# Kernel tuning notes

Measured on AMD Instinct MI355X. Metric: run time of the kernel, lower is better.

## Reference

```python
import jax, jax.numpy as jnp
import numpy as np

NF, NH1, NH21, NH22, NCLS = 6, 128, 128, 128, 3
OBS_X, OBS_Y, OBS_Z, R = 10.0, 10.0, 9.0, 7.0
BATCH = 131072


def setup_inputs() -> dict:
    key = jax.random.key(0)
    ks = jax.random.split(key, 16)
    def lin(kw, kb, fan_in, fan_out):
        bound = 1.0 / np.sqrt(fan_in)
        w = jax.random.uniform(kw, (fan_out, fan_in), jnp.float32, -bound, bound)
        b = jax.random.uniform(kb, (fan_out,), jnp.float32, -bound, bound)
        return w, b
    fc1_w, fc1_b = lin(ks[0], ks[1], NF, NH1)
    fc21_w, fc21_b = lin(ks[2], ks[3], NH1, NH21)
    fc22_w, fc22_b = lin(ks[4], ks[5], NH1, NH22)
    fcm1_w, fcm1_b = lin(ks[6], ks[7], NH21, NH21)
    fcm2_w, fcm2_b = lin(ks[8], ks[9], NH22, NH22)
    fc31_w, fc31_b = lin(ks[10], ks[11], NH21, NCLS)
    fc32_w, fc32_b = lin(ks[12], ks[13], NH22, 2)
    x = jax.random.normal(ks[14], (BATCH, NF), jnp.float32)
    mean = jnp.array([10.0, 0.0, 10.0, 0.0, 9.0, 0.0], jnp.float32)
    std = jnp.array([5.0, 2.0, 5.0, 2.0, 5.0, 2.0], jnp.float32)
    return {"x": x, "mean": mean, "std": std,
            "fc1_w": fc1_w, "fc1_b": fc1_b,
            "fc21_w": fc21_w, "fc21_b": fc21_b,
            "fc22_w": fc22_w, "fc22_b": fc22_b,
            "fcm1_w": fcm1_w, "fcm1_b": fcm1_b,
            "fcm2_w": fcm2_w, "fcm2_b": fcm2_b,
            "fc31_w": fc31_w, "fc31_b": fc31_b,
            "fc32_w": fc32_w, "fc32_b": fc32_b,
            "sgn": 1}


def _forward(x, mean, std, fc1_w, fc1_b, fc21_w, fc21_b, fc22_w, fc22_b,
             fcm1_w, fcm1_b, fcm2_w, fcm2_b, fc31_w, fc31_b, fc32_w, fc32_b):
    x0 = x * std + mean                                   # de-normalized state [B,6]
    h = jnp.tanh(x @ fc1_w.T + fc1_b)                     # [B,NH1]
    x21 = jnp.tanh(h @ fc21_w.T + fc21_b)
    x22 = jnp.tanh(h @ fc22_w.T + fc22_b)
    x21 = jnp.tanh(x21 @ fcm1_w.T + fcm1_b)
    x22 = jnp.tanh(x22 @ fcm2_w.T + fcm2_b)
    x31 = x21 @ fc31_w.T + fc31_b                         # QP linear term p, [B,3]
    x32 = 4.0 * jax.nn.sigmoid(x22 @ fc32_w.T + fc32_b)   # HOCBF penalties, [B,2]

    # higher-order CBF terms
    px, vx, py, vy, pz, vz = (x0[:, i] for i in range(6))
    dx, dy, dz = px - OBS_X, py - OBS_Y, pz - OBS_Z
    barrier = dx**4 + dy**4 + dz**4 - R**4
    barrier_dot = 4.0 * (dx**3 * vx + dy**3 * vy + dz**3 * vz)
    Lf2b = 12.0 * (dx**2 * vx**2 + dy**2 * vy**2 + dz**2 * vz**2)
    G = -4.0 * jnp.stack([dx**3, dy**3, dz**3], axis=-1)  # [B,3], single constraint G u <= h
    hvec = Lf2b + (x32[:, 0] + x32[:, 1]) * barrier_dot + x32[:, 0] * x32[:, 1] * barrier  # [B]

    # QP: min 0.5 u^T u + x31^T u  s.t.  G u <= h  (Q = I, one constraint)
    # Closed-form KKT: u = -x31 - lam*G, lam = max(0, (G @ (-x31) - h) / (G @ G))
    u_unc = -x31
    Gu = jnp.sum(G * u_unc, axis=-1)                      # [B]
    GG = jnp.sum(G * G, axis=-1)                          # [B]
    lam = jnp.maximum(Gu - hvec, 0.0) / GG
    u = u_unc - lam[:, None] * G                          # [B,3]
    return u


def reference(x, mean, std, fc1_w, fc1_b, fc21_w, fc21_b, fc22_w, fc22_b,
              fcm1_w, fcm1_b, fcm2_w, fcm2_b, fc31_w, fc31_b, fc32_w, fc32_b, sgn):
    return _forward(x, mean, std, fc1_w, fc1_b, fc21_w, fc21_b, fc22_w, fc22_b,
                    fcm1_w, fcm1_b, fcm2_w, fcm2_b, fc31_w, fc31_b, fc32_w, fc32_b)
```

## Files before the change

### kernel.cpp

```cpp
#include <hip/hip_runtime.h>

typedef _Float16 half8 __attribute__((ext_vector_type(8)));
typedef _Float16 half4_t __attribute__((ext_vector_type(4)));
typedef float float4_t __attribute__((ext_vector_type(4)));

#define NH 128
#define SB 64
#define NT 256

#define OFF_W1   0
#define OFF_W21  4096
#define OFF_W22  20480
#define OFF_WM1  36864
#define OFF_WM2  53248
#define OFF_W4   69632
#define WS_ELEMS 70272

__device__ __forceinline__ float fast_tanh(float x) {
  x = fminf(15.f, fmaxf(-15.f, x));
  float e = __builtin_amdgcn_exp2f(x * 2.8853900817779268f);
  return (e - 1.f) * __builtin_amdgcn_rcpf(e + 1.f);
}
__device__ __forceinline__ float sigmoid4(float z) {
  z = fminf(30.f, fmaxf(-30.f, z));
  float e = __builtin_amdgcn_exp2f(-z * 1.4426950408889634f);
  return 4.f * __builtin_amdgcn_rcpf(1.f + e);
}

__global__ void prepack(const float* __restrict__ w1, const float* __restrict__ w21,
                        const float* __restrict__ w22, const float* __restrict__ wm1,
                        const float* __restrict__ wm2, const float* __restrict__ w31,
                        const float* __restrict__ w32, _Float16* __restrict__ ws) {
  for (int i = blockIdx.x * blockDim.x + threadIdx.x; i < WS_ELEMS;
       i += gridDim.x * blockDim.x) {
    float v;
    if (i < OFF_W21) {
      int t = i;
      int j = t & 7, c = t >> 3, l16 = c & 15, t1 = c >> 4;
      int k8 = t1 & 3, mt = t1 >> 2;
      int row = mt * 16 + l16, k = k8 * 8 + j;
      v = (k < 6) ? w1[row * 6 + k] : 0.f;
    } else if (i < OFF_W4) {
      int t = i - OFF_W21;
      int m = t >> 14; t &= 16383;
      const float* src = (m == 0) ? w21 : (m == 1) ? w22 : (m == 2) ? wm1 : wm2;
      int j = t & 7, c = t >> 3, l16 = c & 15, t1 = c >> 4;
      int k8 = t1 & 15, mt = t1 >> 4;
      v = src[(mt * 16 + l16) * 128 + k8 * 8 + j];
    } else {
      int t = i - OFF_W4;
      int r = t >> 7, k = t & 127;
      v = (r < 3) ? w31[r * 128 + k] : w32[(r - 3) * 128 + k];
    }
    ws[i] = (_Float16)v;
  }
}

template <int K>
__device__ __forceinline__ void gemm_layer(const _Float16* __restrict__ Wg,
                                           const _Float16* __restrict__ inB,
                                           const float* __restrict__ biasL,
                                           _Float16* __restrict__ outB) {
  constexpr int KC = K / 8;
  constexpr int KS = K / 32;
  const int tid  = threadIdx.x;
  const int wv   = tid >> 6;
  const int lane = tid & 63;
  const int quad = lane >> 4;
  const int l16  = lane & 15;
  const int mt0 = wv * 2, mt1 = mt0 + 1;

  half8 a0[KS], a1[KS];
#pragma unroll
  for (int kk = 0; kk < KS; ++kk) {
    a0[kk] = *(const half8*)(Wg + ((mt0 * KC + kk * 4 + quad) * 16 + l16) * 8);
    a1[kk] = *(const half8*)(Wg + ((mt1 * KC + kk * 4 + quad) * 16 + l16) * 8);
  }
  float4_t acc0[4], acc1[4];
#pragma unroll
  for (int nt = 0; nt < 4; ++nt) {
    acc0[nt] = (float4_t){0.f, 0.f, 0.f, 0.f};
    acc1[nt] = (float4_t){0.f, 0.f, 0.f, 0.f};
  }
#pragma unroll
  for (int kk = 0; kk < KS; ++kk) {
#pragma unroll
    for (int nt = 0; nt < 4; ++nt) {
      half8 b = *(const half8*)(inB + (kk * 4 + quad) * 512 + (nt * 16 + l16) * 8);
      acc0[nt] = __builtin_amdgcn_mfma_f32_16x16x32_f16(a0[kk], b, acc0[nt], 0, 0, 0);
      acc1[nt] = __builtin_amdgcn_mfma_f32_16x16x32_f16(a1[kk], b, acc1[nt], 0, 0, 0);
    }
  }
  const float4_t bv0 = *(const float4_t*)(biasL + mt0 * 16 + quad * 4);
  const float4_t bv1 = *(const float4_t*)(biasL + mt1 * 16 + quad * 4);
  const int ob0 = mt0 * 16 + quad * 4;
  const int ob1 = mt1 * 16 + quad * 4;
#pragma unroll
  for (int nt = 0; nt < 4; ++nt) {
    const int s = nt * 16 + l16;
    half4_t h0, h1;
#pragma unroll
    for (int r = 0; r < 4; ++r) {
      h0[r] = (_Float16)fast_tanh(acc0[nt][r] + bv0[r]);
      h1[r] = (_Float16)fast_tanh(acc1[nt][r] + bv1[r]);
    }
    *(half4_t*)(outB + (ob0 >> 3) * 512 + s * 8 + (ob0 & 7)) = h0;
    *(half4_t*)(outB + (ob1 >> 3) * 512 + s * 8 + (ob1 & 7)) = h1;
  }
}

__global__ __launch_bounds__(NT) void bnet_main(
    const float* __restrict__ x, const float* __restrict__ meang,
    const float* __restrict__ stdg, const float* __restrict__ b1,
    const float* __restrict__ b21, const float* __restrict__ b22,
    const float* __restrict__ bm1, const float* __restrict__ bm2,
    const float* __restrict__ b31, const float* __restrict__ b32,
    const _Float16* __restrict__ ws, float* __restrict__ out) {
  __shared__ __align__(16) _Float16 bufH[SB * NH];
  __shared__ __align__(16) _Float16 bufA[SB * NH];
  __shared__ __align__(16) _Float16 bufB[SB * NH];
  __shared__ __align__(16) _Float16 xb[SB * 32];
  __shared__ __align__(16) float bias_lds[5 * 128];
  __shared__ __align__(16) float part[NT * 5];

  const int tid = threadIdx.x;
  const int s0 = blockIdx.x * SB;

  for (int i = tid; i < 640; i += NT) {
    int layer = i >> 7, idx = i & 127;
    const float* src = (layer == 0) ? b1 : (layer == 1) ? b21
                     : (layer == 2) ? b22 : (layer == 3) ? bm1 : bm2;
    bias_lds[i] = src[idx];
  }
  {
    half8 v;
#pragma unroll
    for (int j = 0; j < 8; ++j) v[j] = (_Float16)0.f;
    if ((tid >> 6) == 0) {
      const float* xp = x + (size_t)(s0 + (tid & 63)) * 6;
#pragma unroll
      for (int j = 0; j < 6; ++j) v[j] = (_Float16)xp[j];
    }
    *(half8*)(xb + tid * 8) = v;
  }
  __syncthreads();

  gemm_layer<32>(ws + OFF_W1, xb, bias_lds, bufH);
  __syncthreads();
  gemm_layer<128>(ws + OFF_W21, bufH, bias_lds + 128, bufA);
  gemm_layer<128>(ws + OFF_W22, bufH, bias_lds + 256, bufB);
  __syncthreads();
  gemm_layer<128>(ws + OFF_WM1, bufA, bias_lds + 384, bufH);
  __syncthreads();
  gemm_layer<128>(ws + OFF_WM2, bufB, bias_lds + 512, bufA);
  __syncthreads();

  {
    const int s = tid & 63, q = tid >> 6;
#pragma unroll
    for (int j = 0; j < 5; ++j) {
      const _Float16* xm = (j < 3) ? bufH : bufA;
      const _Float16* wr = ws + OFF_W4 + j * 128 + q * 32;
      float acc = 0.f;
#pragma unroll
      for (int c = 0; c < 4; ++c) {
        half8 xv = *(const half8*)(xm + (q * 4 + c) * 512 + s * 8);
        half8 wv = *(const half8*)(wr + c * 8);
#pragma unroll
        for (int e = 0; e < 8; ++e) acc += (float)xv[e] * (float)wv[e];
      }
      part[tid * 5 + j] = acc;
    }
  }
  __syncthreads();

  if (tid < SB) {
    const int s = tid;
    float r[5];
#pragma unroll
    for (int j = 0; j < 5; ++j)
      r[j] = part[s * 5 + j] + part[(64 + s) * 5 + j] +
             part[(128 + s) * 5 + j] + part[(192 + s) * 5 + j];
    float u0 = -(r[0] + b31[0]);
    float u1 = -(r[1] + b31[1]);
    float u2 = -(r[2] + b31[2]);
    float p0 = sigmoid4(r[3] + b32[0]);
    float p1 = sigmoid4(r[4] + b32[1]);
    const float* xp = x + (size_t)(s0 + s) * 6;
    float px = xp[0] * stdg[0] + meang[0];
    float vx = xp[1] * stdg[1] + meang[1];
    float py = xp[2] * stdg[2] + meang[2];
    float vy = xp[3] * stdg[3] + meang[3];
    float pz = xp[4] * stdg[4] + meang[4];
    float vz = xp[5] * stdg[5] + meang[5];
    float dx = px - 10.f, dy = py - 10.f, dz = pz - 9.f;
    float dx2 = dx * dx, dy2 = dy * dy, dz2 = dz * dz;
    float dx3 = dx2 * dx, dy3 = dy2 * dy, dz3 = dz2 * dz;
    float barrier = dx3 * dx + dy3 * dy + dz3 * dz - 2401.f;
    float bdot = 4.f * (dx3 * vx + dy3 * vy + dz3 * vz);
    float Lf2b = 12.f * (dx2 * vx * vx + dy2 * vy * vy + dz2 * vz * vz);
    float g0 = -4.f * dx3, g1 = -4.f * dy3, g2 = -4.f * dz3;
    float hv = Lf2b + (p0 + p1) * bdot + p0 * p1 * barrier;
    float Gu = g0 * u0 + g1 * u1 + g2 * u2;
    float GG = g0 * g0 + g1 * g1 + g2 * g2;
    float lam = fmaxf(Gu - hv, 0.f) / GG;
    float* op = out + (size_t)(s0 + s) * 3;
    op[0] = u0 - lam * g0;
    op[1] = u1 - lam * g1;
    op[2] = u2 - lam * g2;
  }
}

extern "C" void kernel_launch(void* const* d_in, const int* in_sizes, int n_in,
                              void* d_out, int out_size, void* d_ws, size_t ws_size,
                              hipStream_t stream) {
  const float* x    = (const float*)d_in[0];
  const float* mean = (const float*)d_in[1];
  const float* stdv = (const float*)d_in[2];
  const float* w1   = (const float*)d_in[3];
  const float* b1   = (const float*)d_in[4];
  const float* w21  = (const float*)d_in[5];
  const float* b21  = (const float*)d_in[6];
  const float* w22  = (const float*)d_in[7];
  const float* b22  = (const float*)d_in[8];
  const float* wm1  = (const float*)d_in[9];
  const float* bm1  = (const float*)d_in[10];
  const float* wm2  = (const float*)d_in[11];
  const float* bm2  = (const float*)d_in[12];
  const float* w31  = (const float*)d_in[13];
  const float* b31  = (const float*)d_in[14];
  const float* w32  = (const float*)d_in[15];
  const float* b32  = (const float*)d_in[16];
  _Float16* ws = (_Float16*)d_ws;
  float* out = (float*)d_out;
  const int batch = in_sizes[0] / 6;

  hipLaunchKernelGGL(prepack, dim3(96), dim3(NT), 0, stream,
                     w1, w21, w22, wm1, wm2, w31, w32, ws);
  hipLaunchKernelGGL(bnet_main, dim3(batch / SB), dim3(NT), 0, stream,
                     x, mean, stdv, b1, b21, b22, bm1, bm2, b31, b32,
                     (const _Float16*)ws, out);
}
```

Baseline: 135.8 us.

## Halve sample tile, move biases to workspace, alias LDS, raise occupancy

```diff
diff --git a/kernel.cpp b/kernel.cpp
--- a/kernel.cpp
+++ b/kernel.cpp
@@ -4,8 +4,7 @@
 typedef _Float16 half4_t __attribute__((ext_vector_type(4)));
 typedef float float4_t __attribute__((ext_vector_type(4)));
 
-#define NH 128
-#define SB 64
+#define SB 32
 #define NT 256
 
 #define OFF_W1   0
@@ -14,15 +13,14 @@
 #define OFF_WM1  36864
 #define OFF_WM2  53248
 #define OFF_W4   69632
-#define WS_ELEMS 70272
+#define OFF_BIAS 70272
+#define WS_WELEMS 70272
 
 __device__ __forceinline__ float fast_tanh(float x) {
-  x = fminf(15.f, fmaxf(-15.f, x));
   float e = __builtin_amdgcn_exp2f(x * 2.8853900817779268f);
-  return (e - 1.f) * __builtin_amdgcn_rcpf(e + 1.f);
+  return fmaf(-2.f, __builtin_amdgcn_rcpf(1.f + e), 1.f);
 }
 __device__ __forceinline__ float sigmoid4(float z) {
-  z = fminf(30.f, fmaxf(-30.f, z));
   float e = __builtin_amdgcn_exp2f(-z * 1.4426950408889634f);
   return 4.f * __builtin_amdgcn_rcpf(1.f + e);
 }
@@ -30,9 +28,12 @@
 __global__ void prepack(const float* __restrict__ w1, const float* __restrict__ w21,
                         const float* __restrict__ w22, const float* __restrict__ wm1,
                         const float* __restrict__ wm2, const float* __restrict__ w31,
-                        const float* __restrict__ w32, _Float16* __restrict__ ws) {
-  for (int i = blockIdx.x * blockDim.x + threadIdx.x; i < WS_ELEMS;
-       i += gridDim.x * blockDim.x) {
+                        const float* __restrict__ w32, const float* __restrict__ b1,
+                        const float* __restrict__ b21, const float* __restrict__ b22,
+                        const float* __restrict__ bm1, const float* __restrict__ bm2,
+                        _Float16* __restrict__ ws) {
+  const int stride = gridDim.x * blockDim.x;
+  for (int i = blockIdx.x * blockDim.x + threadIdx.x; i < WS_WELEMS; i += stride) {
     float v;
     if (i < OFF_W21) {
       int t = i;
@@ -54,15 +55,24 @@
     }
     ws[i] = (_Float16)v;
   }
-}
-
-template <int K>
+  float* bws = (float*)(ws + OFF_BIAS);
+  for (int i = blockIdx.x * blockDim.x + threadIdx.x; i < 640; i += stride) {
+    int layer = i >> 7, idx = i & 127;
+    const float* src = (layer == 0) ? b1 : (layer == 1) ? b21
+                     : (layer == 2) ? b22 : (layer == 3) ? bm1 : bm2;
+    bws[i] = src[idx];
+  }
+}
+
+template <int K, int SBX>
 __device__ __forceinline__ void gemm_layer(const _Float16* __restrict__ Wg,
                                            const _Float16* __restrict__ inB,
-                                           const float* __restrict__ biasL,
+                                           const float* __restrict__ biasG,
                                            _Float16* __restrict__ outB) {
   constexpr int KC = K / 8;
   constexpr int KS = K / 32;
+  constexpr int NTT = SBX / 16;
+  constexpr int RS = SBX * 8;
   const int tid  = threadIdx.x;
   const int wv   = tid >> 6;
   const int lane = tid & 63;
@@ -76,27 +86,27 @@
     a0[kk] = *(const half8*)(Wg + ((mt0 * KC + kk * 4 + quad) * 16 + l16) * 8);
     a1[kk] = *(const half8*)(Wg + ((mt1 * KC + kk * 4 + quad) * 16 + l16) * 8);
   }
-  float4_t acc0[4], acc1[4];
-#pragma unroll
-  for (int nt = 0; nt < 4; ++nt) {
+  float4_t acc0[NTT], acc1[NTT];
+#pragma unroll
+  for (int nt = 0; nt < NTT; ++nt) {
     acc0[nt] = (float4_t){0.f, 0.f, 0.f, 0.f};
     acc1[nt] = (float4_t){0.f, 0.f, 0.f, 0.f};
   }
 #pragma unroll
   for (int kk = 0; kk < KS; ++kk) {
 #pragma unroll
-    for (int nt = 0; nt < 4; ++nt) {
-      half8 b = *(const half8*)(inB + (kk * 4 + quad) * 512 + (nt * 16 + l16) * 8);
+    for (int nt = 0; nt < NTT; ++nt) {
+      half8 b = *(const half8*)(inB + (kk * 4 + quad) * RS + (nt * 16 + l16) * 8);
       acc0[nt] = __builtin_amdgcn_mfma_f32_16x16x32_f16(a0[kk], b, acc0[nt], 0, 0, 0);
       acc1[nt] = __builtin_amdgcn_mfma_f32_16x16x32_f16(a1[kk], b, acc1[nt], 0, 0, 0);
     }
   }
-  const float4_t bv0 = *(const float4_t*)(biasL + mt0 * 16 + quad * 4);
-  const float4_t bv1 = *(const float4_t*)(biasL + mt1 * 16 + quad * 4);
+  const float4_t bv0 = *(const float4_t*)(biasG + mt0 * 16 + quad * 4);
+  const float4_t bv1 = *(const float4_t*)(biasG + mt1 * 16 + quad * 4);
   const int ob0 = mt0 * 16 + quad * 4;
   const int ob1 = mt1 * 16 + quad * 4;
 #pragma unroll
-  for (int nt = 0; nt < 4; ++nt) {
+  for (int nt = 0; nt < NTT; ++nt) {
     const int s = nt * 16 + l16;
     half4_t h0, h1;
 #pragma unroll
@@ -104,73 +114,76 @@
       h0[r] = (_Float16)fast_tanh(acc0[nt][r] + bv0[r]);
       h1[r] = (_Float16)fast_tanh(acc1[nt][r] + bv1[r]);
     }
-    *(half4_t*)(outB + (ob0 >> 3) * 512 + s * 8 + (ob0 & 7)) = h0;
-    *(half4_t*)(outB + (ob1 >> 3) * 512 + s * 8 + (ob1 & 7)) = h1;
-  }
-}
-
-__global__ __launch_bounds__(NT) void bnet_main(
+    *(half4_t*)(outB + (ob0 >> 3) * RS + s * 8 + (ob0 & 7)) = h0;
+    *(half4_t*)(outB + (ob1 >> 3) * RS + s * 8 + (ob1 & 7)) = h1;
+  }
+}
+
+__global__ __launch_bounds__(NT, 5) void bnet_main(
     const float* __restrict__ x, const float* __restrict__ meang,
-    const float* __restrict__ stdg, const float* __restrict__ b1,
-    const float* __restrict__ b21, const float* __restrict__ b22,
-    const float* __restrict__ bm1, const float* __restrict__ bm2,
-    const float* __restrict__ b31, const float* __restrict__ b32,
-    const _Float16* __restrict__ ws, float* __restrict__ out) {
-  __shared__ __align__(16) _Float16 bufH[SB * NH];
-  __shared__ __align__(16) _Float16 bufA[SB * NH];
-  __shared__ __align__(16) _Float16 bufB[SB * NH];
-  __shared__ __align__(16) _Float16 xb[SB * 32];
-  __shared__ __align__(16) float bias_lds[5 * 128];
-  __shared__ __align__(16) float part[NT * 5];
+    const float* __restrict__ stdg, const float* __restrict__ b31,
+    const float* __restrict__ b32, const _Float16* __restrict__ ws,
+    float* __restrict__ out) {
+  __shared__ __align__(16) _Float16 bufH[SB * 128];
+  __shared__ __align__(16) _Float16 bufA[SB * 128];
+  __shared__ __align__(16) _Float16 bufB[SB * 128];
+  __shared__ __align__(16) unsigned char uni[NT * 5 * 4];
+
+  _Float16* xb = (_Float16*)uni;
+  float* part = (float*)uni;
 
   const int tid = threadIdx.x;
   const int s0 = blockIdx.x * SB;
-
-  for (int i = tid; i < 640; i += NT) {
-    int layer = i >> 7, idx = i & 127;
-    const float* src = (layer == 0) ? b1 : (layer == 1) ? b21
-                     : (layer == 2) ? b22 : (layer == 3) ? bm1 : bm2;
-    bias_lds[i] = src[idx];
-  }
+  const float* biasW = (const float*)(ws + OFF_BIAS);
+
+  if (tid < 128) {
+    const int s = tid & 31, k8 = tid >> 5;
+    half8 v;
+#pragma unroll
+    for (int j = 0; j < 8; ++j) v[j] = (_Float16)0.f;
+    if (k8 == 0) {
+      const float* xp = x + (size_t)(s0 + s) * 6;
+#pragma unroll
+      for (int j = 0; j < 6; ++j) v[j] = (_Float16)xp[j];
+    }
+    *(half8*)(xb + k8 * (SB * 8) + s * 8) = v;
+  }
+  __syncthreads();
+
+  gemm_layer<32, SB>(ws + OFF_W1, xb, biasW, bufH);
+  __syncthreads();
+  gemm_layer<128, SB>(ws + OFF_W21, bufH, biasW + 128, bufA);
+  gemm_layer<128, SB>(ws + OFF_W22, bufH, biasW + 256, bufB);
+  __syncthreads();
+  gemm_layer<128, SB>(ws + OFF_WM1, bufA, biasW + 384, bufH);
+  __syncthreads();
+  gemm_layer<128, SB>(ws + OFF_WM2, bufB, biasW + 512, bufA);
+  __syncthreads();
+
   {
-    half8 v;
-#pragma unroll
-    for (int j = 0; j < 8; ++j) v[j] = (_Float16)0.f;
-    if ((tid >> 6) == 0) {
-      const float* xp = x + (size_t)(s0 + (tid & 63)) * 6;
-#pragma unroll
-      for (int j = 0; j < 6; ++j) v[j] = (_Float16)xp[j];
-    }
-    *(half8*)(xb + tid * 8) = v;
-  }
-  __syncthreads();
-
-  gemm_layer<32>(ws + OFF_W1, xb, bias_lds, bufH);
-  __syncthreads();
-  gemm_layer<128>(ws + OFF_W21, bufH, bias_lds + 128, bufA);
-  gemm_layer<128>(ws + OFF_W22, bufH, bias_lds + 256, bufB);
-  __syncthreads();
-  gemm_layer<128>(ws + OFF_WM1, bufA, bias_lds + 384, bufH);
-  __syncthreads();
-  gemm_layer<128>(ws + OFF_WM2, bufB, bias_lds + 512, bufA);
-  __syncthreads();
-
-  {
-    const int s = tid & 63, q = tid >> 6;
+    const int s = tid & 31, q = tid >> 5;
+    half8 xm1a = *(const half8*)(bufH + (2 * q + 0) * (SB * 8) + s * 8);
+    half8 xm1b = *(const half8*)(bufH + (2 * q + 1) * (SB * 8) + s * 8);
+    half8 xm2a = *(const half8*)(bufA + (2 * q + 0) * (SB * 8) + s * 8);
+    half8 xm2b = *(const half8*)(bufA + (2 * q + 1) * (SB * 8) + s * 8);
+    float res[5];
 #pragma unroll
     for (int j = 0; j < 5; ++j) {
-      const _Float16* xm = (j < 3) ? bufH : bufA;
-      const _Float16* wr = ws + OFF_W4 + j * 128 + q * 32;
+      const _Float16* wr = ws + OFF_W4 + j * 128 + q * 16;
+      half8 wa = *(const half8*)(wr);
+      half8 wb = *(const half8*)(wr + 8);
+      half8 xa = (j < 3) ? xm1a : xm2a;
+      half8 xc = (j < 3) ? xm1b : xm2b;
       float acc = 0.f;
 #pragma unroll
-      for (int c = 0; c < 4; ++c) {
-        half8 xv = *(const half8*)(xm + (q * 4 + c) * 512 + s * 8);
-        half8 wv = *(const half8*)(wr + c * 8);
-#pragma unroll
-        for (int e = 0; e < 8; ++e) acc += (float)xv[e] * (float)wv[e];
-      }
-      part[tid * 5 + j] = acc;
-    }
+      for (int e = 0; e < 8; ++e) acc = fmaf((float)xa[e], (float)wa[e], acc);
+#pragma unroll
+      for (int e = 0; e < 8; ++e) acc = fmaf((float)xc[e], (float)wb[e], acc);
+      res[j] = acc;
+    }
+    __syncthreads();
+#pragma unroll
+    for (int j = 0; j < 5; ++j) part[tid * 5 + j] = res[j];
   }
   __syncthreads();
 
@@ -178,9 +191,12 @@
     const int s = tid;
     float r[5];
 #pragma unroll
-    for (int j = 0; j < 5; ++j)
-      r[j] = part[s * 5 + j] + part[(64 + s) * 5 + j] +
-             part[(128 + s) * 5 + j] + part[(192 + s) * 5 + j];
+    for (int j = 0; j < 5; ++j) {
+      float a = 0.f;
+#pragma unroll
+      for (int q = 0; q < 8; ++q) a += part[(q * 32 + s) * 5 + j];
+      r[j] = a;
+    }
     float u0 = -(r[0] + b31[0]);
     float u1 = -(r[1] + b31[1]);
     float u2 = -(r[2] + b31[2]);
@@ -236,8 +252,8 @@
   const int batch = in_sizes[0] / 6;
 
   hipLaunchKernelGGL(prepack, dim3(96), dim3(NT), 0, stream,
-                     w1, w21, w22, wm1, wm2, w31, w32, ws);
+                     w1, w21, w22, wm1, wm2, w31, w32,
+                     b1, b21, b22, bm1, bm2, ws);
   hipLaunchKernelGGL(bnet_main, dim3(batch / SB), dim3(NT), 0, stream,
-                     x, mean, stdv, b1, b21, b22, bm1, bm2, b31, b32,
-                     (const _Float16*)ws, out);
-}
+                     x, mean, stdv, b31, b32, (const _Float16*)ws, out);
+}
```

New measurement: 134.8 us. Within noise of the previous version (-0.8%).
